# Optimization experiments

Hardware: AMD Instinct MI355X
Metric: run time of the kernel (lower is better)

The kernel has to match this reference:

```python
import jax, jax.numpy as jnp
import numpy as np
from jax import lax

RATE, STRIDE, KSIZE, FUSE_K, SCALE = 2, 1, 3, 3, 10.0


def img2col(img, k, s):
    # torch F.unfold with padding=1, reshaped to [B, L, C, k, k] (L row-major over patch grid)
    B, C, H, W = img.shape
    p = jnp.pad(img, ((0, 0), (0, 0), (1, 1), (1, 1)))
    nH = (H + 2 - k) // s + 1
    nW = (W + 2 - k) // s + 1
    slabs = [p[:, :, ki:ki + s * (nH - 1) + 1:s, kj:kj + s * (nW - 1) + 1:s]
             for ki in range(k) for kj in range(k)]
    pats = jnp.stack(slabs, axis=2).reshape(B, C, k, k, nH, nW)
    return pats.transpose(0, 4, 5, 1, 2, 3).reshape(B, nH * nW, C, k, k)


def diag_prop(M, fk):
    # conv2d of the [L, L] score matrix with an identity fuse kernel == sum over diagonal shifts
    r = fk // 2
    B, L, _ = M.shape
    Mp = jnp.pad(M, ((0, 0), (r, r), (r, r)))
    out = jnp.zeros_like(M)
    for d in range(-r, r + 1):
        out = out + Mp[:, r + d:r + d + L, r + d:r + d + L]
    return out


def _fwd(foreground, background, mask):
    pad = KSIZE // 2
    # raw-resolution background patches used for reconstruction: [B, L, C, 2*rate, 2*rate]
    cols = img2col(background, 2 * RATE, RATE * STRIDE)
    # nearest-neighbor downsample by rate (torch F.interpolate scale_factor=1/rate, mode='nearest')
    fg = foreground[:, :, ::RATE, ::RATE]
    bg = background[:, :, ::RATE, ::RATE]
    m = mask[:, :, ::RATE, ::RATE]
    mask_cols = img2col(m, KSIZE, STRIDE)            # [B, L, 1, 3, 3]
    masked = jnp.sum(mask_cols, axis=(2, 3, 4)) == 0.0  # [B, L]
    kern = img2col(bg, KSIZE, STRIDE)                # [B, L, C, 3, 3]
    denom = jnp.sqrt(jnp.sum(kern * kern, axis=(2, 3, 4), keepdims=True))
    kern = kern / jnp.maximum(denom, 1e-3)

    def conv_one(img, k_):  # img [C,h,w], k_ [L,C,3,3] -> [L,h,w]
        return lax.conv_general_dilated(img[None], k_, (1, 1), [(pad, pad), (pad, pad)],
                                        dimension_numbers=('NCHW', 'OIHW', 'NCHW'))[0]

    scores = jax.vmap(conv_one)(fg, kern)            # [B, L, h, w]
    B, L, h, w = scores.shape
    # attention propagation: identity-kernel conv over [h*w, h*w], both orientations
    M = diag_prop(scores.reshape(B, L, h * w), FUSE_K)
    M = M.reshape(B, h, w, h, w).transpose(0, 2, 1, 4, 3).reshape(B, h * w, h * w)
    M = diag_prop(M, FUSE_K)
    scores = M.reshape(B, h, w, h, w).transpose(0, 2, 1, 4, 3).reshape(B, L, h, w)
    scores = jnp.where(masked[:, :, None, None], -1000.0, scores)
    soft = jax.nn.softmax(SCALE * scores, axis=1)

    kt = 2 * RATE
    tpad = kt - 1 - pad  # conv_transpose2d(stride=rate, padding=pad) as dilated conv

    def deconv_one(s_, t_):  # s_ [L,h,w], t_ [L,C,kt,kt] -> [C,H,W]
        W2 = jnp.flip(jnp.transpose(t_, (1, 0, 2, 3)), (2, 3))  # [C,L,kt,kt]
        return lax.conv_general_dilated(s_[None], W2, (1, 1), [(tpad, tpad), (tpad, tpad)],
                                        lhs_dilation=(RATE, RATE),
                                        dimension_numbers=('NCHW', 'OIHW', 'NCHW'))[0]

    return jax.vmap(deconv_one)(soft, cols)          # [B, C, H, W]


def setup_inputs() -> dict:
    key = jax.random.key(0)
    kf, kb, km = jax.random.split(key, 3)
    B, C, H, W = 2, 64, 128, 128
    foreground = jax.random.normal(kf, (B, C, H, W), jnp.float32)
    background = jax.random.normal(kb, (B, C, H, W), jnp.float32)
    mask = (jax.random.uniform(km, (B, 1, H, W)) > 0.5).astype(jnp.float32)
    return {"foreground": foreground, "background": background, "mask": mask}


def reference(foreground, background, mask):
    return _fwd(foreground, background, mask)
```

## Files before the change

### kernel.cpp

```cpp
#include <hip/hip_runtime.h>
#include <hip/hip_bf16.h>

#define B_ 2
#define C_ 64
#define H_ 128
#define W_ 128
#define HS 64
#define WS 64
#define L_ 4096
#define S_ 4096
#define K1_ 576
#define NCOL 1024
#define SCALE_ 10.0f

typedef __attribute__((ext_vector_type(8))) short bf16x8;
typedef __attribute__((ext_vector_type(8))) _Float16 f16x8;
typedef __attribute__((ext_vector_type(4))) float f32x4;

__device__ __forceinline__ void async_copy16(const void* gsrc, void* ldst) {
    __builtin_amdgcn_global_load_lds(
        (__attribute__((address_space(1))) const void*)gsrc,
        (__attribute__((address_space(3))) void*)ldst, 16, 0, 0);
}

__device__ __forceinline__ int TT(int x) { return ((x & 63) << 6) | (x >> 6); }

__device__ __forceinline__ float diag3Y(const float* __restrict__ Y, int l, int s) {
    int tl = TT(l), ts = TT(s);
    float acc = 0.f;
#pragma unroll
    for (int d2 = -1; d2 <= 1; ++d2) {
        int p = tl + d2, q = ts + d2;
        if ((unsigned)p < 4096u && (unsigned)q < 4096u)
            acc += Y[((size_t)TT(p) << 12) + TT(q)];
    }
    return acc;
}

__global__ void k_sumsq(const float* __restrict__ bg, float* __restrict__ ssq) {
    int idx = blockIdx.x * 256 + threadIdx.x;
    if (idx >= B_ * HS * WS) return;
    int pix = idx & 4095, b = idx >> 12;
    int i = pix >> 6, j = pix & 63;
    float ss = 0.f;
    for (int c = 0; c < C_; ++c) {
        float v = bg[((b * C_ + c) * H_ + 2 * i) * W_ + 2 * j];
        ss += v * v;
    }
    ssq[idx] = ss;
}

__global__ void k_patch_stats(const float* __restrict__ mask, const float* __restrict__ ssq,
                              float* __restrict__ denom_inv, float* __restrict__ maskedf) {
    int idx = blockIdx.x * 256 + threadIdx.x;
    if (idx >= B_ * L_) return;
    int b = idx >> 12, l = idx & 4095, lh = l >> 6, lw = l & 63;
    float msum = 0.f, ss = 0.f;
    for (int di = -1; di <= 1; ++di)
        for (int dj = -1; dj <= 1; ++dj) {
            int i = lh + di, j = lw + dj;
            if (i >= 0 && i < HS && j >= 0 && j < WS) {
                msum += mask[(b * H_ + 2 * i) * W_ + 2 * j];
                ss += ssq[(b << 12) + (i << 6) + j];
            }
        }
    maskedf[idx] = (msum == 0.0f) ? 1.0f : 0.0f;
    denom_inv[idx] = 1.0f / fmaxf(sqrtf(ss), 0.001f);
}

__global__ void k_prep(const float* __restrict__ bgb, const float* __restrict__ fgb,
                       _Float16* __restrict__ bcol, _Float16* __restrict__ fcol,
                       __hip_bfloat16* __restrict__ colsT) {
    int idx = blockIdx.x * 256 + threadIdx.x;
    if (idx < 2 * L_ * K1_) {
        int which = idx >= L_ * K1_;
        int id = which ? idx - L_ * K1_ : idx;
        const float* src = which ? fgb : bgb;
        _Float16* dst = which ? fcol : bcol;
        int k = id % K1_;
        int l = id / K1_;
        int c = k / 9, r = k - 9 * c;
        int r3 = r / 3;
        int di = r3 - 1, dj = r - 3 * r3 - 1;
        int i = (l >> 6) + di, j = (l & 63) + dj;
        float v = 0.f;
        if (i >= 0 && i < HS && j >= 0 && j < WS) v = src[(c * H_ + 2 * i) * W_ + 2 * j];
        dst[id] = (_Float16)v;
    } else {
        int id = idx - 2 * L_ * K1_;
        int l = id & 4095, n = id >> 12;
        int kj = n & 3, ki = (n >> 2) & 3, c = n >> 4;
        int y = 2 * (l >> 6) + ki - 1, x = 2 * (l & 63) + kj - 1;
        float v = 0.f;
        if (y >= 0 && y < H_ && x >= 0 && x < W_) v = bgb[(c * H_ + y) * W_ + x];
        colsT[id] = __float2bfloat16(v);
    }
}

__global__ __launch_bounds__(256) void k_gemm1_mfma(const _Float16* __restrict__ A,
                                                    const _Float16* __restrict__ Bm,
                                                    const float* __restrict__ dinv,
                                                    float* __restrict__ scores,
                                                    float* __restrict__ Y) {
    __shared__ __align__(16) char shraw[128 * 129 * 4];
    int t = threadIdx.x, lane = t & 63, w = t >> 6;
    int wm = w & 1, wn = w >> 1;
    int M0 = blockIdx.y * 128, N0 = blockIdx.x * 128;
    f32x4 acc[4][4] = {};

    auto stage = [&](int k0, int offh) {
        _Float16* Asb = (_Float16*)shraw + offh;
        _Float16* Bsb = Asb + 8192;
#pragma unroll
        for (int rp = 0; rp < 4; ++rp) {
            int chunk = rp * 256 + t;
            int row = chunk >> 3;
            int kc = (chunk & 7) ^ (row & 7);
            async_copy16(A + (size_t)(M0 + row) * K1_ + k0 + kc * 8, &Asb[chunk * 8]);
        }
#pragma unroll
        for (int rp = 0; rp < 4; ++rp) {
            int chunk = rp * 256 + t;
            int row = chunk >> 3;
            int kc = (chunk & 7) ^ (row & 7);
            async_copy16(Bm + (size_t)(N0 + row) * K1_ + k0 + kc * 8, &Bsb[chunk * 8]);
        }
    };

    stage(0, 0);
    int buf = 0;
    for (int k0 = 0; k0 < K1_; k0 += 64) {
        if (k0 + 64 < K1_) {
            stage(k0 + 64, (buf ^ 1) * 16384);
            asm volatile("s_waitcnt vmcnt(8)" ::: "memory");
        } else {
            asm volatile("s_waitcnt vmcnt(0)" ::: "memory");
        }
        __builtin_amdgcn_s_barrier();
        _Float16* As = (_Float16*)shraw + buf * 16384;
        _Float16* Bs = As + 8192;
        int qc = lane >> 4, mr = lane & 15;
#pragma unroll
        for (int kk = 0; kk < 2; ++kk) {
            int c = kk * 4 + qc;
            f16x8 af[4], bfr[4];
#pragma unroll
            for (int i = 0; i < 4; ++i) {
                int ra = wm * 64 + i * 16 + mr;
                int rb = wn * 64 + i * 16 + mr;
                af[i] = *(const f16x8*)&As[ra * 64 + (c ^ (ra & 7)) * 8];
                bfr[i] = *(const f16x8*)&Bs[rb * 64 + (c ^ (rb & 7)) * 8];
            }
#pragma unroll
            for (int mt = 0; mt < 4; ++mt)
#pragma unroll
                for (int nt = 0; nt < 4; ++nt)
                    acc[mt][nt] = __builtin_amdgcn_mfma_f32_16x16x32_f16(af[mt], bfr[nt], acc[mt][nt], 0, 0, 0);
        }
        __builtin_amdgcn_s_barrier();
        buf ^= 1;
    }
    int col = lane & 15, rq = (lane >> 4) * 4;
#pragma unroll
    for (int mt = 0; mt < 4; ++mt)
#pragma unroll
        for (int r = 0; r < 4; ++r) {
            int ml = wm * 64 + mt * 16 + rq + r;
            bool rstrip = (ml <= 1) || (ml >= 126);
            float dv = dinv[M0 + ml];
#pragma unroll
            for (int nt = 0; nt < 4; ++nt) {
                int nl = wn * 64 + nt * 16 + col;
                bool cstrip = (nl <= 1) || (nl >= 126);
                if (rstrip || cstrip)
                    scores[((size_t)(M0 + ml) << 12) + N0 + nl] = acc[mt][nt][r] * dv;
            }
        }
    float* sm = (float*)shraw;
#pragma unroll
    for (int mt = 0; mt < 4; ++mt)
#pragma unroll
        for (int r = 0; r < 4; ++r) {
            int ml = wm * 64 + mt * 16 + rq + r;
            float dv = dinv[M0 + ml];
#pragma unroll
            for (int nt = 0; nt < 4; ++nt) {
                int nl = wn * 64 + nt * 16 + col;
                sm[ml * 129 + nl] = acc[mt][nt][r] * dv;
            }
        }
    __syncthreads();
    for (int e = t; e < 126 * 128; e += 256) {
        int rr = 1 + (e >> 7);
        int cc = e & 127;
        if (cc < 1 || cc > 126) continue;
        float y = sm[(rr - 1) * 129 + cc - 1] + sm[rr * 129 + cc] + sm[(rr + 1) * 129 + cc + 1];
        Y[((size_t)(M0 + rr) << 12) + N0 + cc] = y;
    }
}

__global__ void k_pass1_edge(const float* __restrict__ scores, float* __restrict__ Y) {
    int idx = blockIdx.x * 256 + threadIdx.x;
    int a, c;
    if (idx < 262144) {
        int ri = idx >> 12;
        a = (ri >> 1) * 128 + ((ri & 1) ? 127 : 0);
        c = idx & 4095;
    } else {
        int j = idx - 262144;
        int ci = j >> 12;
        c = (ci >> 1) * 128 + ((ci & 1) ? 127 : 0);
        a = j & 4095;
    }
    float acc = 0.f;
#pragma unroll
    for (int d = -1; d <= 1; ++d) {
        int aa = a + d, cc = c + d;
        if ((unsigned)aa < 4096u && (unsigned)cc < 4096u)
            acc += scores[((size_t)aa << 12) + cc];
    }
    Y[((size_t)a << 12) + c] = acc;
}

__global__ __launch_bounds__(256) void k_soft3(const float* __restrict__ Y,
                                               const float* __restrict__ maskedf,
                                               __hip_bfloat16* __restrict__ softT,
                                               float* __restrict__ pml, float* __restrict__ pz) {
    __shared__ float tile[64][65];
    __shared__ float red[16][64];
    __shared__ float mloc[64];
    int t = threadIdx.x;
    int sx4 = t & 15, lg = t >> 4;
    int bid = blockIdx.x;
    int swz = (bid & 7) * 512 + (bid >> 3);
    int dg = swz >> 6, pos = swz & 63;
    int by = pos, bx = (pos + dg) & 63;
    int s0 = bx * 64, l0 = by * 64;
    bool interior = (bx >= 1) && (bx <= 62) && (by >= 1) && (by <= 62);
    float p0 = -3.0e38f, p1 = -3.0e38f, p2 = -3.0e38f, p3 = -3.0e38f;
    if (interior) {
        float4 v[12];
        float mk[4];
#pragma unroll
        for (int j = 0; j < 4; ++j) {
            int lloc = lg + 16 * j;
#pragma unroll
            for (int d2 = 0; d2 < 3; ++d2) {
                const float* p = Y + ((size_t)(64 * (by + d2 - 1) + lloc) << 12) + 64 * (bx + d2 - 1) + 4 * sx4;
                v[j * 3 + d2] = *(const float4*)p;
            }
        }
#pragma unroll
        for (int j = 0; j < 4; ++j) mk[j] = maskedf[l0 + lg + 16 * j];
#pragma unroll
        for (int j = 0; j < 4; ++j) {
            int lloc = lg + 16 * j;
            float a0 = v[j * 3].x + v[j * 3 + 1].x + v[j * 3 + 2].x;
            float a1 = v[j * 3].y + v[j * 3 + 1].y + v[j * 3 + 2].y;
            float a2 = v[j * 3].z + v[j * 3 + 1].z + v[j * 3 + 2].z;
            float a3 = v[j * 3].w + v[j * 3 + 1].w + v[j * 3 + 2].w;
            if (mk[j] != 0.f) { a0 = -1000.f; a1 = -1000.f; a2 = -1000.f; a3 = -1000.f; }
            tile[lloc][4 * sx4 + 0] = a0;
            tile[lloc][4 * sx4 + 1] = a1;
            tile[lloc][4 * sx4 + 2] = a2;
            tile[lloc][4 * sx4 + 3] = a3;
            p0 = fmaxf(p0, a0); p1 = fmaxf(p1, a1); p2 = fmaxf(p2, a2); p3 = fmaxf(p3, a3);
        }
    } else {
#pragma unroll
        for (int j = 0; j < 4; ++j) {
            int lloc = lg + 16 * j;
            int l = l0 + lloc;
            bool mk = (maskedf[l] != 0.f);
            float a0 = mk ? -1000.f : diag3Y(Y, l, s0 + 4 * sx4 + 0);
            float a1 = mk ? -1000.f : diag3Y(Y, l, s0 + 4 * sx4 + 1);
            float a2 = mk ? -1000.f : diag3Y(Y, l, s0 + 4 * sx4 + 2);
            float a3 = mk ? -1000.f : diag3Y(Y, l, s0 + 4 * sx4 + 3);
            tile[lloc][4 * sx4 + 0] = a0;
            tile[lloc][4 * sx4 + 1] = a1;
            tile[lloc][4 * sx4 + 2] = a2;
            tile[lloc][4 * sx4 + 3] = a3;
            p0 = fmaxf(p0, a0); p1 = fmaxf(p1, a1); p2 = fmaxf(p2, a2); p3 = fmaxf(p3, a3);
        }
    }
    red[lg][4 * sx4 + 0] = p0;
    red[lg][4 * sx4 + 1] = p1;
    red[lg][4 * sx4 + 2] = p2;
    red[lg][4 * sx4 + 3] = p3;
    __syncthreads();
    if (t < 64) {
        float m = -3.0e38f;
#pragma unroll
        for (int g = 0; g < 16; ++g) m = fmaxf(m, red[g][t]);
        mloc[t] = m;
        pml[(size_t)(s0 + t) * 64 + by] = m;
    }
    __syncthreads();
    float m0 = mloc[4 * sx4 + 0], m1 = mloc[4 * sx4 + 1], m2 = mloc[4 * sx4 + 2], m3 = mloc[4 * sx4 + 3];
    float z0 = 0.f, z1 = 0.f, z2 = 0.f, z3 = 0.f;
#pragma unroll
    for (int j = 0; j < 4; ++j) {
        int lloc = lg + 16 * j;
        float e0 = __expf(SCALE_ * (tile[lloc][4 * sx4 + 0] - m0));
        float e1 = __expf(SCALE_ * (tile[lloc][4 * sx4 + 1] - m1));
        float e2 = __expf(SCALE_ * (tile[lloc][4 * sx4 + 2] - m2));
        float e3 = __expf(SCALE_ * (tile[lloc][4 * sx4 + 3] - m3));
        tile[lloc][4 * sx4 + 0] = e0;
        tile[lloc][4 * sx4 + 1] = e1;
        tile[lloc][4 * sx4 + 2] = e2;
        tile[lloc][4 * sx4 + 3] = e3;
        z0 += e0; z1 += e1; z2 += e2; z3 += e3;
    }
    red[lg][4 * sx4 + 0] = z0;
    red[lg][4 * sx4 + 1] = z1;
    red[lg][4 * sx4 + 2] = z2;
    red[lg][4 * sx4 + 3] = z3;
    __syncthreads();
    if (t < 64) {
        float zz = 0.f;
#pragma unroll
        for (int g = 0; g < 16; ++g) zz += red[g][t];
        pz[(size_t)(s0 + t) * 64 + by] = zz;
    }
#pragma unroll
    for (int pp = 0; pp < 2; ++pp) {
        int chunk = pp * 256 + t;
        int sloc = chunk >> 3, lb = (chunk & 7) * 8;
        bf16x8 o;
#pragma unroll
        for (int k = 0; k < 8; ++k) {
            __hip_bfloat16 r = __float2bfloat16(tile[lb + k][sloc]);
            o[k] = *reinterpret_cast<short*>(&r);
        }
        *(bf16x8*)(softT + ((size_t)(s0 + sloc) << 12) + l0 + lb) = o;
    }
}

__global__ __launch_bounds__(256) void k_zr(const float* __restrict__ pml,
                                            const float* __restrict__ pz,
                                            __hip_bfloat16* __restrict__ softT) {
    __shared__ float facs[64];
    int t = threadIdx.x;
    int s = blockIdx.x;
    if (t < 64) {
        float pmv = pml[(size_t)s * 64 + t];
        float m = pmv;
#pragma unroll
        for (int off = 1; off < 64; off <<= 1) m = fmaxf(m, __shfl_xor(m, off));
        float fc = __expf(SCALE_ * (pmv - m));
        float g = pz[(size_t)s * 64 + t] * fc;
#pragma unroll
        for (int off = 1; off < 64; off <<= 1) g += __shfl_xor(g, off);
        facs[t] = fc * (1.0f / g);
    }
    __syncthreads();
    size_t rowbase = (size_t)s << 12;
#pragma unroll
    for (int p = 0; p < 2; ++p) {
        int chunk = t + p * 256;
        float f = facs[chunk >> 3];
        bf16x8 v = *(const bf16x8*)(softT + rowbase + chunk * 8);
        bf16x8 o;
#pragma unroll
        for (int k = 0; k < 8; ++k) {
            unsigned short us = (unsigned short)v[k];
            float x = __uint_as_float((unsigned)us << 16) * f;
            __hip_bfloat16 r = __float2bfloat16(x);
            o[k] = *reinterpret_cast<short*>(&r);
        }
        *(bf16x8*)(softT + rowbase + chunk * 8) = o;
    }
}

__global__ __launch_bounds__(256) void k_gemm2_mfma(const __hip_bfloat16* __restrict__ softT,
                                                    const __hip_bfloat16* __restrict__ colsT,
                                                    float* __restrict__ patchP) {
    __shared__ __hip_bfloat16 AsB[2][16384];
    int t = threadIdx.x, lane = t & 63, w = t >> 6;
    int wm = w & 1, wn = w >> 1;
    int flat = blockIdx.x + (blockIdx.y << 3) + (blockIdx.z << 8);
    int swz = (flat & 7) * 64 + (flat >> 3);
    int zp = swz >> 8;
    int rem = swz & 255;
    int yp = rem >> 3, xp = rem & 7;
    int M0 = yp * 128, N0 = xp * 128;
    int kbase = zp * 2048;
    f32x4 acc[4][4] = {};

    auto stage = [&](int k0, int bsel) {
        __hip_bfloat16* Asb = AsB[bsel];
        __hip_bfloat16* Bsb = Asb + 8192;
#pragma unroll
        for (int rp = 0; rp < 4; ++rp) {
            int chunk = rp * 256 + t;
            int row = chunk >> 3;
            int kc = (chunk & 7) ^ (row & 7);
            async_copy16(softT + ((size_t)(M0 + row) << 12) + k0 + kc * 8, &Asb[chunk * 8]);
        }
#pragma unroll
        for (int rp = 0; rp < 4; ++rp) {
            int chunk = rp * 256 + t;
            int row = chunk >> 3;
            int kc = (chunk & 7) ^ (row & 7);
            async_copy16(colsT + ((size_t)(N0 + row) << 12) + k0 + kc * 8, &Bsb[chunk * 8]);
        }
    };

    stage(kbase, 0);
    int buf = 0;
    for (int k0 = kbase; k0 < kbase + 2048; k0 += 64) {
        if (k0 + 64 < kbase + 2048) {
            stage(k0 + 64, buf ^ 1);
            asm volatile("s_waitcnt vmcnt(8)" ::: "memory");
        } else {
            asm volatile("s_waitcnt vmcnt(0)" ::: "memory");
        }
        __builtin_amdgcn_s_barrier();
        __hip_bfloat16* As = AsB[buf];
        __hip_bfloat16* Bs = As + 8192;
        int qc = lane >> 4, mr = lane & 15;
#pragma unroll
        for (int kk = 0; kk < 2; ++kk) {
            int c = kk * 4 + qc;
            bf16x8 af[4], bfr[4];
#pragma unroll
            for (int i = 0; i < 4; ++i) {
                int rowa = wm * 64 + i * 16 + mr;
                af[i] = *(const bf16x8*)&As[rowa * 64 + (c ^ (rowa & 7)) * 8];
                int rowb = wn * 64 + i * 16 + mr;
                bfr[i] = *(const bf16x8*)&Bs[rowb * 64 + (c ^ (rowb & 7)) * 8];
            }
#pragma unroll
            for (int mt = 0; mt < 4; ++mt)
#pragma unroll
                for (int nt = 0; nt < 4; ++nt)
                    acc[mt][nt] = __builtin_amdgcn_mfma_f32_16x16x32_bf16(af[mt], bfr[nt], acc[mt][nt], 0, 0, 0);
        }
        __builtin_amdgcn_s_barrier();
        buf ^= 1;
    }
    float* P = patchP + ((size_t)zp << 22);
    int col = lane & 15, rq = (lane >> 4) * 4;
#pragma unroll
    for (int mt = 0; mt < 4; ++mt) {
        int m0 = M0 + wm * 64 + mt * 16 + rq;
#pragma unroll
        for (int nt = 0; nt < 4; ++nt) {
            int n = N0 + wn * 64 + nt * 16 + col;
            *(f32x4*)&P[(size_t)n * 4096 + m0] = acc[mt][nt];
        }
    }
}

__global__ void k_col2im(const float* __restrict__ patchP, float* __restrict__ outb) {
    int idx = blockIdx.x * 256 + threadIdx.x;
    if (idx >= C_ * H_ * W_) return;
    int x = idx & 127, y = (idx >> 7) & 127, c = idx >> 14;
    const float* P0 = patchP;
    const float* P1 = patchP + (1u << 22);
    float acc = 0.f;
    int ki0 = (y + 1) & 1, kj0 = (x + 1) & 1;
#pragma unroll
    for (int ki = ki0; ki < 4; ki += 2) {
        int i = (y + 1 - ki) >> 1;
        if (i < 0 || i >= HS) continue;
#pragma unroll
        for (int kj = kj0; kj < 4; kj += 2) {
            int j = (x + 1 - kj) >> 1;
            if (j < 0 || j >= WS) continue;
            size_t off = ((size_t)(c * 16 + ki * 4 + kj) << 12) + i * 64 + j;
            acc += P0[off] + P1[off];
        }
    }
    outb[idx] = acc;
}

extern "C" void kernel_launch(void* const* d_in, const int* in_sizes, int n_in,
                              void* d_out, int out_size, void* d_ws, size_t ws_size,
                              hipStream_t stream) {
    (void)in_sizes; (void)n_in; (void)out_size; (void)ws_size;
    const float* fg = (const float*)d_in[0];
    const float* bg = (const float*)d_in[1];
    const float* mask = (const float*)d_in[2];
    float* out = (float*)d_out;

    float* ws = (float*)d_ws;
    float* scores = ws;
    float* patchP = ws;
    float* Y = ws + 16777216;
    _Float16* bgcol = (_Float16*)(ws + 33554432);
    _Float16* fgcol = (_Float16*)(ws + 34734080);
    __hip_bfloat16* softT = (__hip_bfloat16*)(ws + 38273024);
    __hip_bfloat16* colsT = (__hip_bfloat16*)(ws + 46661632);
    float* pml = ws + 48758784;
    float* pz = ws + 49020928;
    float* denom_inv = ws + 49283072;
    float* maskedf = ws + 49291264;
    float* ssq = ws + 49299456;

    k_sumsq<<<(B_ * HS * WS) / 256, 256, 0, stream>>>(bg, ssq);
    k_patch_stats<<<(B_ * L_) / 256, 256, 0, stream>>>(mask, ssq, denom_inv, maskedf);

    for (int b = 0; b < B_; ++b) {
        const float* bgb = bg + (size_t)b * C_ * H_ * W_;
        const float* fgb = fg + (size_t)b * C_ * H_ * W_;

        k_prep<<<(2 * L_ * K1_ + NCOL * L_) / 256, 256, 0, stream>>>(bgb, fgb, bgcol, fgcol, colsT);

        dim3 g1(32, 32);
        k_gemm1_mfma<<<g1, 256, 0, stream>>>(bgcol, fgcol, denom_inv + b * L_, scores, Y);
        k_pass1_edge<<<2048, 256, 0, stream>>>(scores, Y);

        k_soft3<<<4096, 256, 0, stream>>>(Y, maskedf + b * L_, softT, pml, pz);
        k_zr<<<4096, 256, 0, stream>>>(pml, pz, softT);

        dim3 g5(8, 32, 2);
        k_gemm2_mfma<<<g5, 256, 0, stream>>>(softT, colsT, patchP);
        k_col2im<<<(C_ * H_ * W_) / 256, 256, 0, stream>>>(patchP, out + (size_t)b * C_ * H_ * W_);
    }
}
```

Baseline: 399.9 us.

## Fuse both diagonal propagation passes into softmax kernel, drop Y intermediate

Removes the first diagonal-sum pass from the GEMM epilogue and the edge-fix kernel, so the GEMM writes the full scaled score matrix and skips the LDS staging and Y writes. The softmax kernel then computes the 3x3 diagonal propagation directly from scores with nine unaligned float4 loads per output group, and the interior test is narrowed to keep neighbouring tiles in range. This drops a 64MB intermediate write and read plus one launch per batch. In exchange, the softmax kernel issues three times as many global loads, and they are unaligned, so it relies on cache hits.

New measurement: 413.6 us. 3.4% more time.

```diff
diff --git a/kernel.cpp b/kernel.cpp
--- a/kernel.cpp
+++ b/kernel.cpp
@@ -25,14 +25,26 @@
 
 __device__ __forceinline__ int TT(int x) { return ((x & 63) << 6) | (x >> 6); }
 
-__device__ __forceinline__ float diag3Y(const float* __restrict__ Y, int l, int s) {
+__device__ __forceinline__ float4 ld4u(const float* p) {
+    float4 v;
+    __builtin_memcpy(&v, p, sizeof(float4));
+    return v;
+}
+
+__device__ __forceinline__ float diag9(const float* __restrict__ S, int l, int s) {
     int tl = TT(l), ts = TT(s);
     float acc = 0.f;
 #pragma unroll
     for (int d2 = -1; d2 <= 1; ++d2) {
         int p = tl + d2, q = ts + d2;
-        if ((unsigned)p < 4096u && (unsigned)q < 4096u)
-            acc += Y[((size_t)TT(p) << 12) + TT(q)];
+        if ((unsigned)p >= 4096u || (unsigned)q >= 4096u) continue;
+        int a = TT(p), c = TT(q);
+#pragma unroll
+        for (int d1 = -1; d1 <= 1; ++d1) {
+            int aa = a + d1, cc = c + d1;
+            if ((unsigned)aa < 4096u && (unsigned)cc < 4096u)
+                acc += S[((size_t)aa << 12) + cc];
+        }
     }
     return acc;
 }
@@ -100,16 +112,15 @@
 __global__ __launch_bounds__(256) void k_gemm1_mfma(const _Float16* __restrict__ A,
                                                     const _Float16* __restrict__ Bm,
                                                     const float* __restrict__ dinv,
-                                                    float* __restrict__ scores,
-                                                    float* __restrict__ Y) {
-    __shared__ __align__(16) char shraw[128 * 129 * 4];
+                                                    float* __restrict__ scores) {
+    __shared__ __align__(16) _Float16 AsB[2][16384];
     int t = threadIdx.x, lane = t & 63, w = t >> 6;
     int wm = w & 1, wn = w >> 1;
     int M0 = blockIdx.y * 128, N0 = blockIdx.x * 128;
     f32x4 acc[4][4] = {};
 
-    auto stage = [&](int k0, int offh) {
-        _Float16* Asb = (_Float16*)shraw + offh;
+    auto stage = [&](int k0, int bsel) {
+        _Float16* Asb = AsB[bsel];
         _Float16* Bsb = Asb + 8192;
 #pragma unroll
         for (int rp = 0; rp < 4; ++rp) {
@@ -131,13 +142,13 @@
     int buf = 0;
     for (int k0 = 0; k0 < K1_; k0 += 64) {
         if (k0 + 64 < K1_) {
-            stage(k0 + 64, (buf ^ 1) * 16384);
+            stage(k0 + 64, buf ^ 1);
             asm volatile("s_waitcnt vmcnt(8)" ::: "memory");
         } else {
             asm volatile("s_waitcnt vmcnt(0)" ::: "memory");
         }
         __builtin_amdgcn_s_barrier();
-        _Float16* As = (_Float16*)shraw + buf * 16384;
+        _Float16* As = AsB[buf];
         _Float16* Bs = As + 8192;
         int qc = lane >> 4, mr = lane & 15;
 #pragma unroll
@@ -166,63 +177,16 @@
 #pragma unroll
         for (int r = 0; r < 4; ++r) {
             int ml = wm * 64 + mt * 16 + rq + r;
-            bool rstrip = (ml <= 1) || (ml >= 126);
             float dv = dinv[M0 + ml];
 #pragma unroll
             for (int nt = 0; nt < 4; ++nt) {
                 int nl = wn * 64 + nt * 16 + col;
-                bool cstrip = (nl <= 1) || (nl >= 126);
-                if (rstrip || cstrip)
-                    scores[((size_t)(M0 + ml) << 12) + N0 + nl] = acc[mt][nt][r] * dv;
+                scores[((size_t)(M0 + ml) << 12) + N0 + nl] = acc[mt][nt][r] * dv;
             }
         }
-    float* sm = (float*)shraw;
-#pragma unroll
-    for (int mt = 0; mt < 4; ++mt)
-#pragma unroll
-        for (int r = 0; r < 4; ++r) {
-            int ml = wm * 64 + mt * 16 + rq + r;
-            float dv = dinv[M0 + ml];
-#pragma unroll
-            for (int nt = 0; nt < 4; ++nt) {
-                int nl = wn * 64 + nt * 16 + col;
-                sm[ml * 129 + nl] = acc[mt][nt][r] * dv;
-            }
-        }
-    __syncthreads();
-    for (int e = t; e < 126 * 128; e += 256) {
-        int rr = 1 + (e >> 7);
-        int cc = e & 127;
-        if (cc < 1 || cc > 126) continue;
-        float y = sm[(rr - 1) * 129 + cc - 1] + sm[rr * 129 + cc] + sm[(rr + 1) * 129 + cc + 1];
-        Y[((size_t)(M0 + rr) << 12) + N0 + cc] = y;
-    }
-}
-
-__global__ void k_pass1_edge(const float* __restrict__ scores, float* __restrict__ Y) {
-    int idx = blockIdx.x * 256 + threadIdx.x;
-    int a, c;
-    if (idx < 262144) {
-        int ri = idx >> 12;
-        a = (ri >> 1) * 128 + ((ri & 1) ? 127 : 0);
-        c = idx & 4095;
-    } else {
-        int j = idx - 262144;
-        int ci = j >> 12;
-        c = (ci >> 1) * 128 + ((ci & 1) ? 127 : 0);
-        a = j & 4095;
-    }
-    float acc = 0.f;
-#pragma unroll
-    for (int d = -1; d <= 1; ++d) {
-        int aa = a + d, cc = c + d;
-        if ((unsigned)aa < 4096u && (unsigned)cc < 4096u)
-            acc += scores[((size_t)aa << 12) + cc];
-    }
-    Y[((size_t)a << 12) + c] = acc;
-}
-
-__global__ __launch_bounds__(256) void k_soft3(const float* __restrict__ Y,
+}
+
+__global__ __launch_bounds__(256) void k_soft3(const float* __restrict__ S,
                                                const float* __restrict__ maskedf,
                                                __hip_bfloat16* __restrict__ softT,
                                                float* __restrict__ pml, float* __restrict__ pz) {
@@ -236,29 +200,25 @@
     int dg = swz >> 6, pos = swz & 63;
     int by = pos, bx = (pos + dg) & 63;
     int s0 = bx * 64, l0 = by * 64;
-    bool interior = (bx >= 1) && (bx <= 62) && (by >= 1) && (by <= 62);
+    bool interior = (bx >= 2) && (bx <= 61) && (by >= 2) && (by <= 61);
     float p0 = -3.0e38f, p1 = -3.0e38f, p2 = -3.0e38f, p3 = -3.0e38f;
     if (interior) {
-        float4 v[12];
         float mk[4];
+#pragma unroll
+        for (int j = 0; j < 4; ++j) mk[j] = maskedf[l0 + lg + 16 * j];
 #pragma unroll
         for (int j = 0; j < 4; ++j) {
             int lloc = lg + 16 * j;
-#pragma unroll
-            for (int d2 = 0; d2 < 3; ++d2) {
-                const float* p = Y + ((size_t)(64 * (by + d2 - 1) + lloc) << 12) + 64 * (bx + d2 - 1) + 4 * sx4;
-                v[j * 3 + d2] = *(const float4*)p;
-            }
-        }
-#pragma unroll
-        for (int j = 0; j < 4; ++j) mk[j] = maskedf[l0 + lg + 16 * j];
-#pragma unroll
-        for (int j = 0; j < 4; ++j) {
-            int lloc = lg + 16 * j;
-            float a0 = v[j * 3].x + v[j * 3 + 1].x + v[j * 3 + 2].x;
-            float a1 = v[j * 3].y + v[j * 3 + 1].y + v[j * 3 + 2].y;
-            float a2 = v[j * 3].z + v[j * 3 + 1].z + v[j * 3 + 2].z;
-            float a3 = v[j * 3].w + v[j * 3 + 1].w + v[j * 3 + 2].w;
+            const float* base = S + ((size_t)(l0 + lloc) << 12) + s0 + 4 * sx4;
+            float4 v[9];
+#pragma unroll
+            for (int o2 = 0; o2 < 3; ++o2)
+#pragma unroll
+                for (int o1 = 0; o1 < 3; ++o1)
+                    v[o2 * 3 + o1] = ld4u(base + (ptrdiff_t)(64 * (o2 - 1) + (o1 - 1)) * 4097);
+            float a0 = 0.f, a1 = 0.f, a2 = 0.f, a3 = 0.f;
+#pragma unroll
+            for (int i = 0; i < 9; ++i) { a0 += v[i].x; a1 += v[i].y; a2 += v[i].z; a3 += v[i].w; }
             if (mk[j] != 0.f) { a0 = -1000.f; a1 = -1000.f; a2 = -1000.f; a3 = -1000.f; }
             tile[lloc][4 * sx4 + 0] = a0;
             tile[lloc][4 * sx4 + 1] = a1;
@@ -272,10 +232,10 @@
             int lloc = lg + 16 * j;
             int l = l0 + lloc;
             bool mk = (maskedf[l] != 0.f);
-            float a0 = mk ? -1000.f : diag3Y(Y, l, s0 + 4 * sx4 + 0);
-            float a1 = mk ? -1000.f : diag3Y(Y, l, s0 + 4 * sx4 + 1);
-            float a2 = mk ? -1000.f : diag3Y(Y, l, s0 + 4 * sx4 + 2);
-            float a3 = mk ? -1000.f : diag3Y(Y, l, s0 + 4 * sx4 + 3);
+            float a0 = mk ? -1000.f : diag9(S, l, s0 + 4 * sx4 + 0);
+            float a1 = mk ? -1000.f : diag9(S, l, s0 + 4 * sx4 + 1);
+            float a2 = mk ? -1000.f : diag9(S, l, s0 + 4 * sx4 + 2);
+            float a3 = mk ? -1000.f : diag9(S, l, s0 + 4 * sx4 + 3);
             tile[lloc][4 * sx4 + 0] = a0;
             tile[lloc][4 * sx4 + 1] = a1;
             tile[lloc][4 * sx4 + 2] = a2;
@@ -487,7 +447,6 @@
     float* ws = (float*)d_ws;
     float* scores = ws;
     float* patchP = ws;
-    float* Y = ws + 16777216;
     _Float16* bgcol = (_Float16*)(ws + 33554432);
     _Float16* fgcol = (_Float16*)(ws + 34734080);
     __hip_bfloat16* softT = (__hip_bfloat16*)(ws + 38273024);
@@ -508,10 +467,9 @@
         k_prep<<<(2 * L_ * K1_ + NCOL * L_) / 256, 256, 0, stream>>>(bgb, fgb, bgcol, fgcol, colsT);
 
         dim3 g1(32, 32);
-        k_gemm1_mfma<<<g1, 256, 0, stream>>>(bgcol, fgcol, denom_inv + b * L_, scores, Y);
-        k_pass1_edge<<<2048, 256, 0, stream>>>(scores, Y);
-
-        k_soft3<<<4096, 256, 0, stream>>>(Y, maskedf + b * L_, softT, pml, pz);
+        k_gemm1_mfma<<<g1, 256, 0, stream>>>(bgcol, fgcol, denom_inv + b * L_, scores);
+
+        k_soft3<<<4096, 256, 0, stream>>>(scores, maskedf + b * L_, softT, pml, pz);
         k_zr<<<4096, 256, 0, stream>>>(pml, pz, softT);
 
         dim3 g5(8, 32, 2);
```

## Fold softmax normalization factors into gemm2 A-operand and drop rescale pass

Applied to the files above, without the earlier changes.

Replaces the k_zr pass, which re-read and re-wrote the whole 4096x4096 softT matrix to apply per-block softmax correction factors, with a small k_facs kernel that only computes the factors. The factors are staged into shared memory in gemm2 and multiplied into the A fragments before each MFMA. To make that multiply cheap and precise enough, softT and colsT switch from bf16 to fp16 and gemm2 uses the f16 MFMA. This removes a full read-modify-write of the 32 MB softT buffer per batch. In exchange it adds per-fragment multiplies in the inner loop and the risk of fp16 overflow or underflow in unnormalized exp values.

Measured after the change: 387.0 us. 3.2% less time.

```diff
diff --git a/kernel.cpp b/kernel.cpp
--- a/kernel.cpp
+++ b/kernel.cpp
@@ -70,7 +70,7 @@
 
 __global__ void k_prep(const float* __restrict__ bgb, const float* __restrict__ fgb,
                        _Float16* __restrict__ bcol, _Float16* __restrict__ fcol,
-                       __hip_bfloat16* __restrict__ colsT) {
+                       _Float16* __restrict__ colsT) {
     int idx = blockIdx.x * 256 + threadIdx.x;
     if (idx < 2 * L_ * K1_) {
         int which = idx >= L_ * K1_;
@@ -93,7 +93,7 @@
         int y = 2 * (l >> 6) + ki - 1, x = 2 * (l & 63) + kj - 1;
         float v = 0.f;
         if (y >= 0 && y < H_ && x >= 0 && x < W_) v = bgb[(c * H_ + y) * W_ + x];
-        colsT[id] = __float2bfloat16(v);
+        colsT[id] = (_Float16)v;
     }
 }
 
@@ -224,7 +224,7 @@
 
 __global__ __launch_bounds__(256) void k_soft3(const float* __restrict__ Y,
                                                const float* __restrict__ maskedf,
-                                               __hip_bfloat16* __restrict__ softT,
+                                               _Float16* __restrict__ softT,
                                                float* __restrict__ pml, float* __restrict__ pz) {
     __shared__ float tile[64][65];
     __shared__ float red[16][64];
@@ -326,56 +326,34 @@
     for (int pp = 0; pp < 2; ++pp) {
         int chunk = pp * 256 + t;
         int sloc = chunk >> 3, lb = (chunk & 7) * 8;
-        bf16x8 o;
-#pragma unroll
-        for (int k = 0; k < 8; ++k) {
-            __hip_bfloat16 r = __float2bfloat16(tile[lb + k][sloc]);
-            o[k] = *reinterpret_cast<short*>(&r);
-        }
-        *(bf16x8*)(softT + ((size_t)(s0 + sloc) << 12) + l0 + lb) = o;
-    }
-}
-
-__global__ __launch_bounds__(256) void k_zr(const float* __restrict__ pml,
-                                            const float* __restrict__ pz,
-                                            __hip_bfloat16* __restrict__ softT) {
-    __shared__ float facs[64];
-    int t = threadIdx.x;
-    int s = blockIdx.x;
-    if (t < 64) {
-        float pmv = pml[(size_t)s * 64 + t];
-        float m = pmv;
-#pragma unroll
-        for (int off = 1; off < 64; off <<= 1) m = fmaxf(m, __shfl_xor(m, off));
-        float fc = __expf(SCALE_ * (pmv - m));
-        float g = pz[(size_t)s * 64 + t] * fc;
-#pragma unroll
-        for (int off = 1; off < 64; off <<= 1) g += __shfl_xor(g, off);
-        facs[t] = fc * (1.0f / g);
-    }
-    __syncthreads();
-    size_t rowbase = (size_t)s << 12;
-#pragma unroll
-    for (int p = 0; p < 2; ++p) {
-        int chunk = t + p * 256;
-        float f = facs[chunk >> 3];
-        bf16x8 v = *(const bf16x8*)(softT + rowbase + chunk * 8);
-        bf16x8 o;
-#pragma unroll
-        for (int k = 0; k < 8; ++k) {
-            unsigned short us = (unsigned short)v[k];
-            float x = __uint_as_float((unsigned)us << 16) * f;
-            __hip_bfloat16 r = __float2bfloat16(x);
-            o[k] = *reinterpret_cast<short*>(&r);
-        }
-        *(bf16x8*)(softT + rowbase + chunk * 8) = o;
-    }
-}
-
-__global__ __launch_bounds__(256) void k_gemm2_mfma(const __hip_bfloat16* __restrict__ softT,
-                                                    const __hip_bfloat16* __restrict__ colsT,
+        f16x8 o;
+#pragma unroll
+        for (int k = 0; k < 8; ++k) o[k] = (_Float16)tile[lb + k][sloc];
+        *(f16x8*)(softT + ((size_t)(s0 + sloc) << 12) + l0 + lb) = o;
+    }
+}
+
+__global__ __launch_bounds__(256) void k_facs(float* __restrict__ pml,
+                                              const float* __restrict__ pz) {
+    int t = threadIdx.x & 63;
+    int s = blockIdx.x * 4 + (threadIdx.x >> 6);
+    float pmv = pml[(size_t)s * 64 + t];
+    float m = pmv;
+#pragma unroll
+    for (int off = 1; off < 64; off <<= 1) m = fmaxf(m, __shfl_xor(m, off));
+    float fc = __expf(SCALE_ * (pmv - m));
+    float g = pz[(size_t)s * 64 + t] * fc;
+#pragma unroll
+    for (int off = 1; off < 64; off <<= 1) g += __shfl_xor(g, off);
+    pml[(size_t)s * 64 + t] = fc * (1.0f / g);
+}
+
+__global__ __launch_bounds__(256) void k_gemm2_mfma(const _Float16* __restrict__ softT,
+                                                    const _Float16* __restrict__ colsT,
+                                                    const float* __restrict__ facs,
                                                     float* __restrict__ patchP) {
-    __shared__ __hip_bfloat16 AsB[2][16384];
+    __shared__ _Float16 AsB[2][16384];
+    __shared__ _Float16 facH[128 * 33];
     int t = threadIdx.x, lane = t & 63, w = t >> 6;
     int wm = w & 1, wn = w >> 1;
     int flat = blockIdx.x + (blockIdx.y << 3) + (blockIdx.z << 8);
@@ -388,8 +366,8 @@
     f32x4 acc[4][4] = {};
 
     auto stage = [&](int k0, int bsel) {
-        __hip_bfloat16* Asb = AsB[bsel];
-        __hip_bfloat16* Bsb = Asb + 8192;
+        _Float16* Asb = AsB[bsel];
+        _Float16* Bsb = Asb + 8192;
 #pragma unroll
         for (int rp = 0; rp < 4; ++rp) {
             int chunk = rp * 256 + t;
@@ -407,7 +385,15 @@
     };
 
     stage(kbase, 0);
+#pragma unroll
+    for (int it = 0; it < 16; ++it) {
+        int task = it * 256 + t;
+        int row = task >> 5, lb = task & 31;
+        facH[row * 33 + lb] = (_Float16)facs[((size_t)(M0 + row) << 6) | (zp * 32 + lb)];
+    }
+    __syncthreads();
     int buf = 0;
+    int qc = lane >> 4, mr = lane & 15;
     for (int k0 = kbase; k0 < kbase + 2048; k0 += 64) {
         if (k0 + 64 < kbase + 2048) {
             stage(k0 + 64, buf ^ 1);
@@ -416,25 +402,30 @@
             asm volatile("s_waitcnt vmcnt(0)" ::: "memory");
         }
         __builtin_amdgcn_s_barrier();
-        __hip_bfloat16* As = AsB[buf];
-        __hip_bfloat16* Bs = As + 8192;
-        int qc = lane >> 4, mr = lane & 15;
+        _Float16* As = AsB[buf];
+        _Float16* Bs = As + 8192;
+        int lbi = (k0 - kbase) >> 6;
+        _Float16 fh[4];
+#pragma unroll
+        for (int i = 0; i < 4; ++i) fh[i] = facH[(wm * 64 + i * 16 + mr) * 33 + lbi];
 #pragma unroll
         for (int kk = 0; kk < 2; ++kk) {
             int c = kk * 4 + qc;
-            bf16x8 af[4], bfr[4];
+            f16x8 af[4], bfr[4];
 #pragma unroll
             for (int i = 0; i < 4; ++i) {
                 int rowa = wm * 64 + i * 16 + mr;
-                af[i] = *(const bf16x8*)&As[rowa * 64 + (c ^ (rowa & 7)) * 8];
+                af[i] = *(const f16x8*)&As[rowa * 64 + (c ^ (rowa & 7)) * 8];
+#pragma unroll
+                for (int u = 0; u < 8; ++u) af[i][u] *= fh[i];
                 int rowb = wn * 64 + i * 16 + mr;
-                bfr[i] = *(const bf16x8*)&Bs[rowb * 64 + (c ^ (rowb & 7)) * 8];
+                bfr[i] = *(const f16x8*)&Bs[rowb * 64 + (c ^ (rowb & 7)) * 8];
             }
 #pragma unroll
             for (int mt = 0; mt < 4; ++mt)
 #pragma unroll
                 for (int nt = 0; nt < 4; ++nt)
-                    acc[mt][nt] = __builtin_amdgcn_mfma_f32_16x16x32_bf16(af[mt], bfr[nt], acc[mt][nt], 0, 0, 0);
+                    acc[mt][nt] = __builtin_amdgcn_mfma_f32_16x16x32_f16(af[mt], bfr[nt], acc[mt][nt], 0, 0, 0);
         }
         __builtin_amdgcn_s_barrier();
         buf ^= 1;
@@ -490,8 +481,8 @@
     float* Y = ws + 16777216;
     _Float16* bgcol = (_Float16*)(ws + 33554432);
     _Float16* fgcol = (_Float16*)(ws + 34734080);
-    __hip_bfloat16* softT = (__hip_bfloat16*)(ws + 38273024);
-    __hip_bfloat16* colsT = (__hip_bfloat16*)(ws + 46661632);
+    _Float16* softT = (_Float16*)(ws + 38273024);
+    _Float16* colsT = (_Float16*)(ws + 46661632);
     float* pml = ws + 48758784;
     float* pz = ws + 49020928;
     float* denom_inv = ws + 49283072;
@@ -512,10 +503,10 @@
         k_pass1_edge<<<2048, 256, 0, stream>>>(scores, Y);
 
         k_soft3<<<4096, 256, 0, stream>>>(Y, maskedf + b * L_, softT, pml, pz);
-        k_zr<<<4096, 256, 0, stream>>>(pml, pz, softT);
+        k_facs<<<1024, 256, 0, stream>>>(pml, pz);
 
         dim3 g5(8, 32, 2);
-        k_gemm2_mfma<<<g5, 256, 0, stream>>>(softT, colsT, patchP);
+        k_gemm2_mfma<<<g5, 256, 0, stream>>>(softT, colsT, pml, patchP);
         k_col2im<<<(C_ * H_ * W_) / 256, 256, 0, stream>>>(patchP, out + (size_t)b * C_ * H_ * W_);
     }
 }
```
